# Kernel optimization log

Hardware: AMD Instinct MI355X
Metric: run time of the kernel (lower is better)

The kernel has to match this reference:

```python
import jax, jax.numpy as jnp
import numpy as np

B, TE, TD, HE, HD = 16, 512, 64, 512, 512


def setup_inputs() -> dict:
    key = jax.random.key(0)
    k1, k2, k3, k4, k5 = jax.random.split(key, 5)
    return {
        "encoder_out_seq": jax.random.normal(k1, (B, TE, HE), dtype=jnp.float32),
        "decoder_out_seq": jax.random.normal(k2, (B, TD, HD), dtype=jnp.float32),
        "W_a": jax.random.normal(k3, (HE, HE), dtype=jnp.float32) * 0.05,
        "U_a": jax.random.normal(k4, (HD, HE), dtype=jnp.float32) * 0.05,
        "V_a": jax.random.normal(k5, (HE, 1), dtype=jnp.float32) * 0.05,
    }


def reference(encoder_out_seq, decoder_out_seq, W_a, U_a, V_a):
    # Bahdanau additive attention, batched over all decoder steps at once
    # (the original K.rnn loop over Td is embarrassingly parallel).
    Ws = jnp.einsum('bte,eh->bth', encoder_out_seq, W_a)   # [B,Te,He]
    Uh = jnp.einsum('bdk,kh->bdh', decoder_out_seq, U_a)   # [B,Td,He]
    # additive combine + tanh: [B,Td,Te,He]
    act = jnp.tanh(Ws[:, None, :, :] + Uh[:, :, None, :])
    e = jnp.einsum('bdth,h->bdt', act, V_a[:, 0])          # [B,Td,Te]
    e = jax.nn.softmax(e, axis=-1)                          # attention weights
    c = jnp.einsum('bdt,bth->bdh', e, encoder_out_seq)      # [B,Td,He] context
    return (c, e)
```

## Files before the change

kernel.cpp:

```cpp
#include <hip/hip_runtime.h>
#include <hip/hip_bf16.h>

#define BB 16
#define TE 512
#define TD 64
#define HE 512

#define PRESCALE 2.8853900817779268f

typedef __attribute__((ext_vector_type(8))) short bf16x8;
typedef __attribute__((ext_vector_type(4))) float f32x4;

__device__ __forceinline__ float fexp2(float x) {
#if __has_builtin(__builtin_amdgcn_exp2f)
    return __builtin_amdgcn_exp2f(x);
#else
    return exp2f(x);
#endif
}
__device__ __forceinline__ float frcp(float x) {
#if __has_builtin(__builtin_amdgcn_rcpf)
    return __builtin_amdgcn_rcpf(x);
#else
    return __fdividef(1.f, x);
#endif
}

__device__ __forceinline__ void split2(float x, unsigned short& h, unsigned short& l) {
    __hip_bfloat16 hb = __float2bfloat16(x);
    h = *(unsigned short*)&hb;
    float r = x - __bfloat162float(hb);
    __hip_bfloat16 lb = __float2bfloat16(r);
    l = *(unsigned short*)&lb;
}

__device__ __forceinline__ void gload16(const unsigned short* g, void* l) {
    __builtin_amdgcn_global_load_lds(
        (const __attribute__((address_space(1))) unsigned int*)g,
        (__attribute__((address_space(3))) unsigned int*)l, 16, 0, 0);
}



__device__ __forceinline__ void tile_load(const float* __restrict__ src, int ld,
                                          float (*tile)[64], int tid)
{
#pragma unroll
    for (int p = 0; p < 4; ++p) {
        const int f = p * 256 + tid;
        const int r = f >> 4, c4 = f & 15;
        const float4 v = *(const float4*)&src[(size_t)r * ld + c4 * 4];
        *(float4*)&tile[r][((c4 ^ (r & 7))) << 2] = v;
    }
}

__device__ __forceinline__ void tile_outA(float (*tile)[64],
                                          unsigned short* __restrict__ H,
                                          unsigned short* __restrict__ L,
                                          size_t Ms, size_t sg_base, size_t m_base, int tid)
{
#pragma unroll
    for (int p = 0; p < 2; ++p) {
        const int task = p * 256 + tid;
        const int s = task >> 6, mm = task & 63;
        const float4 x = *(const float4*)&tile[mm][(((s << 1)    ) ^ (mm & 7)) << 2];
        const float4 y = *(const float4*)&tile[mm][(((s << 1) | 1) ^ (mm & 7)) << 2];
        ushort4 ha, la, hb, lb;
        split2(x.x, ha.x, la.x); split2(x.y, ha.y, la.y);
        split2(x.z, ha.z, la.z); split2(x.w, ha.w, la.w);
        split2(y.x, hb.x, lb.x); split2(y.y, hb.y, lb.y);
        split2(y.z, hb.z, lb.z); split2(y.w, hb.w, lb.w);
        const size_t o = ((sg_base + s) * Ms + m_base + mm) * 8;
        *(ushort4*)&H[o] = ha; *(ushort4*)&H[o + 4] = hb;
        *(ushort4*)&L[o] = la; *(ushort4*)&L[o + 4] = lb;
    }
}

__device__ __forceinline__ void tile_outT(float (*tile)[64],
                                          unsigned short* __restrict__ H,
                                          unsigned short* __restrict__ L,
                                          size_t Ns, size_t sg_base, size_t n_base, int tid)
{
#pragma unroll
    for (int p = 0; p < 2; ++p) {
        const int task = p * 256 + tid;
        const int s2 = task >> 6, hh = task & 63;
        float v[8];
#pragma unroll
        for (int q = 0; q < 8; ++q) {
            const int r = s2 * 8 + q;
            v[q] = tile[r][((((hh >> 2)) ^ (r & 7)) << 2) + (hh & 3)];
        }
        ushort4 ha, la, hb, lb;
        split2(v[0], ha.x, la.x); split2(v[1], ha.y, la.y);
        split2(v[2], ha.z, la.z); split2(v[3], ha.w, la.w);
        split2(v[4], hb.x, lb.x); split2(v[5], hb.y, lb.y);
        split2(v[6], hb.z, lb.z); split2(v[7], hb.w, lb.w);
        const size_t o = ((sg_base + s2) * Ns + n_base + hh) * 8;
        *(ushort4*)&H[o] = ha; *(ushort4*)&H[o + 4] = hb;
        *(ushort4*)&L[o] = la; *(ushort4*)&L[o + 4] = lb;
    }
}

__global__ __launch_bounds__(256)
void split_all(const float* __restrict__ enc,
               unsigned short* __restrict__ eAh, unsigned short* __restrict__ eAl,
               unsigned short* __restrict__ eTh, unsigned short* __restrict__ eTl,
               const float* __restrict__ dec,
               unsigned short* __restrict__ dH, unsigned short* __restrict__ dL,
               const float* __restrict__ Wa,
               unsigned short* __restrict__ wH, unsigned short* __restrict__ wL,
               const float* __restrict__ Ua,
               unsigned short* __restrict__ uH, unsigned short* __restrict__ uL)
{
    __shared__ float tile[64][64];
    const int tid = threadIdx.x;
    const int x = blockIdx.x, y = blockIdx.y, z = blockIdx.z;

    if (z < 16) {
        if (y < 8) {
            const int h0 = x * 64, t0 = y * 64;
            const size_t bo = (size_t)z * TE * HE;
            tile_load(enc + bo + (size_t)t0 * HE + h0, HE, tile, tid);
            __syncthreads();
            tile_outA(tile, eAh, eAl, (size_t)BB * TE, h0 >> 3, (size_t)z * TE + t0, tid);
            tile_outT(tile, eTh + bo, eTl + bo, HE, t0 >> 3, h0, tid);
        } else if (y == 8) {
            const int m0 = z * 64, h0 = x * 64;
            tile_load(dec + (size_t)m0 * HE + h0, HE, tile, tid);
            __syncthreads();
            tile_outA(tile, dH, dL, (size_t)BB * TD, h0 >> 3, m0, tid);
        }
        return;
    }
    const int yy = (y < 8) ? y : y - 8;
    const float* X = (y < 8) ? Wa : Ua;
    unsigned short* H = (y < 8) ? wH : uH;
    unsigned short* L = (y < 8) ? wL : uL;
    const int r0 = yy * 64, c0 = x * 64;
    tile_load(X + (size_t)r0 * HE + c0, HE, tile, tid);
    __syncthreads();
    tile_outT(tile, H, L, HE, r0 >> 3, c0, tid);
}

#define GEMM_BODY(AH, AL, BH, BL, CPTR, MM, NN, KK, ROW0, COL0, EPI)          \
    f32x4 acc[4][2];                                                           \
    _Pragma("unroll") for (int mi = 0; mi < 4; ++mi)                           \
        _Pragma("unroll") for (int ni = 0; ni < 2; ++ni)                       \
            acc[mi][ni] = (f32x4){0.f, 0.f, 0.f, 0.f};                         \
    auto STAGE = [&](int buf, int k0) {                                        \
        const int sg = k0 >> 3;                                                \
        _Pragma("unroll") for (int c = 0; c < 2; ++c) {                        \
            const int task = c * 256 + tid;                                    \
            const int g = task >> 7, idx = task & 127;                         \
            int mrow = (ROW0) + idx; if (mrow >= (MM)) mrow -= (MM);           \
            const size_t ao = ((size_t)(sg + g) * (MM) + mrow) * 8;            \
            gload16((AH) + ao, smem[buf] + task * 16);                         \
            gload16((AL) + ao, smem[buf] + 8192 + task * 16);                  \
        }                                                                      \
        {                                                                      \
            const int g = tid >> 6, idx = tid & 63;                            \
            const size_t bo = ((size_t)(sg + g) * (NN) + (COL0) + idx) * 8;    \
            gload16((BH) + bo, smem[buf] + 16384 + tid * 16);                  \
            gload16((BL) + bo, smem[buf] + 20480 + tid * 16);                  \
        }                                                                      \
    };                                                                         \
    STAGE(0, 0);                                                               \
    int buf = 0;                                                               \
    for (int k0 = 0; k0 < (KK); k0 += 32) {                                    \
        if (k0 + 32 < (KK)) {                                                  \
            STAGE(buf ^ 1, k0 + 32);                                           \
            asm volatile("s_waitcnt vmcnt(6)\n\ts_barrier" ::: "memory");      \
        } else {                                                               \
            asm volatile("s_waitcnt vmcnt(0)\n\ts_barrier" ::: "memory");      \
        }                                                                      \
        bf16x8 ah[4], al[4], bh[2], bl[2];                                     \
        _Pragma("unroll") for (int mi = 0; mi < 4; ++mi) {                     \
            const int off = (fg * 128 + wr * 64 + mi * 16 + fr) * 16;          \
            ah[mi] = *(const bf16x8*)(smem[buf] + off);                        \
            al[mi] = *(const bf16x8*)(smem[buf] + 8192 + off);                 \
        }                                                                      \
        _Pragma("unroll") for (int ni = 0; ni < 2; ++ni) {                     \
            const int off = (fg * 64 + wc * 32 + ni * 16 + fr) * 16;           \
            bh[ni] = *(const bf16x8*)(smem[buf] + 16384 + off);                \
            bl[ni] = *(const bf16x8*)(smem[buf] + 20480 + off);                \
        }                                                                      \
        _Pragma("unroll") for (int mi = 0; mi < 4; ++mi)                       \
            _Pragma("unroll") for (int ni = 0; ni < 2; ++ni) {                 \
                acc[mi][ni] = __builtin_amdgcn_mfma_f32_16x16x32_bf16(ah[mi], bh[ni], acc[mi][ni], 0, 0, 0); \
                acc[mi][ni] = __builtin_amdgcn_mfma_f32_16x16x32_bf16(ah[mi], bl[ni], acc[mi][ni], 0, 0, 0); \
                acc[mi][ni] = __builtin_amdgcn_mfma_f32_16x16x32_bf16(al[mi], bh[ni], acc[mi][ni], 0, 0, 0); \
            }                                                                  \
        asm volatile("s_barrier" ::: "memory");                                \
        buf ^= 1;                                                              \
    }                                                                          \
    _Pragma("unroll") for (int mi = 0; mi < 4; ++mi) {                         \
        const int rbase = (ROW0) + wr * 64 + mi * 16 + fg * 4;                 \
        _Pragma("unroll") for (int ni = 0; ni < 2; ++ni) {                     \
            const int col = (COL0) + wc * 32 + ni * 16 + fr;                   \
            _Pragma("unroll") for (int r = 0; r < 4; ++r) {                    \
                const int row = rbase + r;                                     \
                if (row < (MM)) { float val = EPI(acc[mi][ni][r]);             \
                    (CPTR)[(size_t)row * (NN) + col] = val; }                  \
            }                                                                  \
        }                                                                      \
    }

#define EPI_EXP2(v) fexp2((v) * PRESCALE)
#define EPI_ID(v)   (v)

__global__ __launch_bounds__(256)
void gemm_ws_uh(const unsigned short* __restrict__ eAh, const unsigned short* __restrict__ eAl,
                const unsigned short* __restrict__ wBh, const unsigned short* __restrict__ wBl,
                float* __restrict__ Ew,
                const unsigned short* __restrict__ dAh, const unsigned short* __restrict__ dAl,
                const unsigned short* __restrict__ uBh, const unsigned short* __restrict__ uBl,
                float* __restrict__ Eu)
{
    __shared__ char smem[2][24576];
    const int tid  = threadIdx.x;
    const int lane = tid & 63;
    const int wave = tid >> 6;
    const int wr = wave >> 1, wc = wave & 1;
    const int fr = lane & 15, fg = lane >> 4;

    const unsigned short *Ahi, *Alo, *Bhi, *Blo;
    float* C;
    int M, row0;
    if (blockIdx.y < 64) {
        Ahi = eAh; Alo = eAl; Bhi = wBh; Blo = wBl; C = Ew;
        M = BB * TE; row0 = blockIdx.y * 128;
    } else {
        Ahi = dAh; Alo = dAl; Bhi = uBh; Blo = uBl; C = Eu;
        M = BB * TD; row0 = (blockIdx.y - 64) * 128;
    }
    const int N = HE, K = HE;
    const int col0 = blockIdx.x * 64;

    GEMM_BODY(Ahi, Alo, Bhi, Blo, C, M, N, K, row0, col0, EPI_EXP2)
}

__global__ __launch_bounds__(256)
void gemm_ctx(const unsigned short* __restrict__ Ahi_, const unsigned short* __restrict__ Alo_,
              const unsigned short* __restrict__ Bhi_, const unsigned short* __restrict__ Blo_,
              float* __restrict__ C_, int M, int N, int K,
              long long sA, long long sB, long long sC)
{
    __shared__ char smem[2][24576];
    const int tid  = threadIdx.x;
    const int lane = tid & 63;
    const int wave = tid >> 6;
    const int wr = wave >> 1, wc = wave & 1;
    const int fr = lane & 15, fg = lane >> 4;
    const int row0 = blockIdx.y * 128;
    const int col0 = blockIdx.x * 64;

    const unsigned short* Ahi = Ahi_ + (size_t)blockIdx.z * sA;
    const unsigned short* Alo = Alo_ + (size_t)blockIdx.z * sA;
    const unsigned short* Bhi = Bhi_ + (size_t)blockIdx.z * sB;
    const unsigned short* Blo = Blo_ + (size_t)blockIdx.z * sB;
    float* C = C_ + (size_t)blockIdx.z * sC;

    GEMM_BODY(Ahi, Alo, Bhi, Blo, C, M, N, K, row0, col0, EPI_ID)
}

__global__ __launch_bounds__(256)
void gemm_f32(const float* __restrict__ A, const float* __restrict__ Bm,
              float* __restrict__ C, int M, int N, int K,
              long long sAb, long long sBb, long long sCb, float scale, int emode)
{
    __shared__ float As[16][68];
    __shared__ float Bs[16][68];

    const int tid = threadIdx.x;
    const int tx  = tid & 15;
    const int ty  = tid >> 4;
    const int row0 = blockIdx.y * 64;
    const int col0 = blockIdx.x * 64;

    A  += (long long)blockIdx.z * sAb;
    Bm += (long long)blockIdx.z * sBb;
    C  += (long long)blockIdx.z * sCb;

    float acc[4][4] = {};

    for (int k0 = 0; k0 < K; k0 += 16) {
        {
            const int r = tid >> 2;
            const int c = (tid & 3) * 4;
            const float4 av = *(const float4*)&A[(long long)(row0 + r) * K + k0 + c];
            As[c + 0][r] = av.x; As[c + 1][r] = av.y;
            As[c + 2][r] = av.z; As[c + 3][r] = av.w;
        }
        {
            const int r = tid >> 4;
            const int c = (tid & 15) * 4;
            *(float4*)&Bs[r][c] = *(const float4*)&Bm[(long long)(k0 + r) * N + col0 + c];
        }
        __syncthreads();

#pragma unroll
        for (int kk = 0; kk < 16; ++kk) {
            const float4 a = *(const float4*)&As[kk][ty * 4];
            const float4 b = *(const float4*)&Bs[kk][tx * 4];
            acc[0][0] += a.x * b.x; acc[0][1] += a.x * b.y; acc[0][2] += a.x * b.z; acc[0][3] += a.x * b.w;
            acc[1][0] += a.y * b.x; acc[1][1] += a.y * b.y; acc[1][2] += a.y * b.z; acc[1][3] += a.y * b.w;
            acc[2][0] += a.z * b.x; acc[2][1] += a.z * b.y; acc[2][2] += a.z * b.z; acc[2][3] += a.z * b.w;
            acc[3][0] += a.w * b.x; acc[3][1] += a.w * b.y; acc[3][2] += a.w * b.z; acc[3][3] += a.w * b.w;
        }
        __syncthreads();
    }

#pragma unroll
    for (int i = 0; i < 4; ++i) {
        float4 o;
        o.x = acc[i][0] * scale; o.y = acc[i][1] * scale;
        o.z = acc[i][2] * scale; o.w = acc[i][3] * scale;
        if (emode) { o.x = fexp2(o.x); o.y = fexp2(o.y); o.z = fexp2(o.z); o.w = fexp2(o.w); }
        *(float4*)&C[(long long)(row0 + ty * 4 + i) * N + col0 + tx * 4] = o;
    }
}

__global__ __launch_bounds__(256)
void scores_raw(const float* __restrict__ Ew, const float* __restrict__ Eu,
                const float* __restrict__ V, float* __restrict__ part)
{
    __shared__ float Ws_s[32][64];
    __shared__ float Uh_s[32][64];
    __shared__ float Vr_s[HE];

    const int tid = threadIdx.x;
    const int tg  = tid & 7;
    const int dg  = tid >> 3;

    const int tt0  = blockIdx.x * 32;
    const int quar = blockIdx.y & 3;
    const int d0   = (blockIdx.y >> 2) * 32;
    const int b    = blockIdx.z;

    const float* Wsg = Ew + (long long)b * TE * HE;
    const float* Uhg = Eu + ((long long)b * TD + d0) * HE;

    if (tid < 128) {
        const float4 v = *(const float4*)&V[tid * 4];
        float4 o; o.x = -2.f * v.x; o.y = -2.f * v.y; o.z = -2.f * v.z; o.w = -2.f * v.w;
        *(float4*)&Vr_s[tid * 4] = o;
    }

    float acc[4] = {0.f, 0.f, 0.f, 0.f};
    const int wswz = tg & 7;
    const int uswz = dg & 7;
    const int hbase = quar * (HE / 4);

    for (int hc = hbase; hc < hbase + HE / 4; hc += 64) {
        __syncthreads();
#pragma unroll
        for (int k = 0; k < 2; ++k) {
            const int idx = tid + k * 256;
            const int r   = idx >> 4;
            const int c4  = idx & 15;
            const float4 wv = *(const float4*)&Wsg[(long long)(tt0 + r) * HE + hc + c4 * 4];
            *(float4*)&Ws_s[r][(c4 ^ ((r >> 2) & 7)) * 4] = wv;
            const float4 uv = *(const float4*)&Uhg[(long long)r * HE + hc + c4 * 4];
            *(float4*)&Uh_s[r][(c4 ^ (r & 7)) * 4] = uv;
        }
        __syncthreads();

#pragma unroll 4
        for (int hs = 0; hs < 64; hs += 4) {
            const int h4 = hs >> 2;
            const float4 vv = *(const float4*)&Vr_s[hc + hs];
            const float4 u  = *(const float4*)&Uh_s[dg][(h4 ^ uswz) * 4];
#pragma unroll
            for (int i = 0; i < 4; ++i) {
                const float4 w = *(const float4*)&Ws_s[tg * 4 + i][(h4 ^ wswz) * 4];
                acc[i] = fmaf(vv.x, frcp(fmaf(w.x, u.x, 1.f)), acc[i]);
                acc[i] = fmaf(vv.y, frcp(fmaf(w.y, u.y, 1.f)), acc[i]);
                acc[i] = fmaf(vv.z, frcp(fmaf(w.z, u.z, 1.f)), acc[i]);
                acc[i] = fmaf(vv.w, frcp(fmaf(w.w, u.w, 1.f)), acc[i]);
            }
        }
    }

    float* dst = part + (size_t)quar * (BB * TD * TE);
    float4 o; o.x = acc[0]; o.y = acc[1]; o.z = acc[2]; o.w = acc[3];
    *(float4*)&dst[((long long)b * TD + d0 + dg) * TE + tt0 + tg * 4] = o;
}

__global__ __launch_bounds__(256)
void softmax_rows(const float* __restrict__ part, float* __restrict__ e,
                  unsigned short* __restrict__ H, unsigned short* __restrict__ L)
{
    const int lane = threadIdx.x & 63;
    const int wave = threadIdx.x >> 6;
    const long long row = blockIdx.x * 4 + wave;

    float4 a = {0.f, 0.f, 0.f, 0.f}, c = {0.f, 0.f, 0.f, 0.f};
#pragma unroll
    for (int q = 0; q < 4; ++q) {
        const float* p = part + (size_t)q * (BB * TD * TE) + row * TE;
        const float4 aq = *(const float4*)&p[lane * 4];
        const float4 cq = *(const float4*)&p[lane * 4 + 256];
        a.x += aq.x; a.y += aq.y; a.z += aq.z; a.w += aq.w;
        c.x += cq.x; c.y += cq.y; c.z += cq.z; c.w += cq.w;
    }

    float m = fmaxf(fmaxf(fmaxf(a.x, a.y), fmaxf(a.z, a.w)),
                    fmaxf(fmaxf(c.x, c.y), fmaxf(c.z, c.w)));
#pragma unroll
    for (int off = 32; off; off >>= 1) m = fmaxf(m, __shfl_xor(m, off));

    a.x = __expf(a.x - m); a.y = __expf(a.y - m); a.z = __expf(a.z - m); a.w = __expf(a.w - m);
    c.x = __expf(c.x - m); c.y = __expf(c.y - m); c.z = __expf(c.z - m); c.w = __expf(c.w - m);

    float s = (a.x + a.y + a.z + a.w) + (c.x + c.y + c.z + c.w);
#pragma unroll
    for (int off = 32; off; off >>= 1) s += __shfl_xor(s, off);

    const float inv = __fdividef(1.f, s);
    a.x *= inv; a.y *= inv; a.z *= inv; a.w *= inv;
    c.x *= inv; c.y *= inv; c.z *= inv; c.w *= inv;
    float* pe = e + row * TE;
    *(float4*)&pe[lane * 4] = a;
    *(float4*)&pe[lane * 4 + 256] = c;

    if (H) {
        const int b = (int)(row >> 6);
        const int d = (int)(row & 63);
        const size_t base = (size_t)b * (TD * TE);
        ushort4 h, l;
        {
            const int t0 = lane * 4;
            const size_t o = base + ((size_t)(t0 >> 3) * TD + d) * 8 + (t0 & 7);
            split2(a.x, h.x, l.x); split2(a.y, h.y, l.y);
            split2(a.z, h.z, l.z); split2(a.w, h.w, l.w);
            *(ushort4*)&H[o] = h;
            *(ushort4*)&L[o] = l;
        }
        {
            const int t0 = lane * 4 + 256;
            const size_t o = base + ((size_t)(t0 >> 3) * TD + d) * 8 + (t0 & 7);
            split2(c.x, h.x, l.x); split2(c.y, h.y, l.y);
            split2(c.z, h.z, l.z); split2(c.w, h.w, l.w);
            *(ushort4*)&H[o] = h;
            *(ushort4*)&L[o] = l;
        }
    }
}

extern "C" void kernel_launch(void* const* d_in, const int* in_sizes, int n_in,
                              void* d_out, int out_size, void* d_ws, size_t ws_size,
                              hipStream_t stream)
{
    const float* enc = (const float*)d_in[0];
    const float* dec = (const float*)d_in[1];
    const float* Wa  = (const float*)d_in[2];
    const float* Ua  = (const float*)d_in[3];
    const float* Va  = (const float*)d_in[4];

    float* out   = (float*)d_out;
    float* c_out = out;
    float* e_out = out + (size_t)BB * TD * HE;

    char* w = (char*)d_ws;
    float* Ew  = (float*)(w);
    float* Eu  = (float*)(w + 16777216);
    unsigned short* encAh = (unsigned short*)(w + 18874368);
    unsigned short* encAl = (unsigned short*)(w + 27262976);
    unsigned short* encTh = (unsigned short*)(w + 35651584);
    unsigned short* encTl = (unsigned short*)(w + 44040192);
    unsigned short* decAh = (unsigned short*)(w + 52428800);
    unsigned short* decAl = (unsigned short*)(w + 53477376);
    unsigned short* WaTh  = (unsigned short*)(w + 54525952);
    unsigned short* WaTl  = (unsigned short*)(w + 55050240);
    unsigned short* UaTh  = (unsigned short*)(w + 55574528);
    unsigned short* UaTl  = (unsigned short*)(w + 56098816);
    unsigned short* eh    = (unsigned short*)(w + 56623104);
    unsigned short* el    = (unsigned short*)(w + 57671680);
    float* part = (float*)(w + 58720256);
    const size_t REQUIRED = 67108864;

    dim3 blk(256);

    if (ws_size >= REQUIRED) {
        split_all<<<dim3(8, 16, 17), blk, 0, stream>>>(
            enc, encAh, encAl, encTh, encTl,
            dec, decAh, decAl, Wa, WaTh, WaTl, Ua, UaTh, UaTl);

        gemm_ws_uh<<<dim3(8, 72, 1), blk, 0, stream>>>(
            encAh, encAl, WaTh, WaTl, Ew, decAh, decAl, UaTh, UaTl, Eu);

        scores_raw<<<dim3(TE / 32, (TD / 32) * 4, BB), blk, 0, stream>>>(Ew, Eu, Va, part);
        softmax_rows<<<dim3(BB * TD / 4), blk, 0, stream>>>(part, e_out, eh, el);

        gemm_ctx<<<dim3(8, 1, BB), blk, 0, stream>>>(
            eh, el, encTh, encTl, c_out, TD, HE, TE,
            (long long)TD * TE, (long long)TE * HE, (long long)TD * HE);
    } else {
        float* pf = (float*)(w + 18874368);
        gemm_f32<<<dim3(HE / 64, (BB * TE) / 64, 1), blk, 0, stream>>>(
            enc, Wa, Ew, BB * TE, HE, HE, 0, 0, 0, PRESCALE, 1);
        gemm_f32<<<dim3(HE / 64, (BB * TD) / 64, 1), blk, 0, stream>>>(
            dec, Ua, Eu, BB * TD, HE, HE, 0, 0, 0, PRESCALE, 1);
        scores_raw<<<dim3(TE / 32, (TD / 32) * 4, BB), blk, 0, stream>>>(Ew, Eu, Va, pf);
        softmax_rows<<<dim3(BB * TD / 4), blk, 0, stream>>>(pf, e_out, nullptr, nullptr);
        gemm_f32<<<dim3(HE / 64, TD / 64, BB), blk, 0, stream>>>(
            e_out, enc, c_out, TD, HE, TE,
            (long long)TD * TE, (long long)TE * HE, (long long)TD * HE, 1.0f, 0);
    }
}
```

Measured before the change: 90.63 us.

## Fuse all stages into one cooperative persistent kernel with grid syncs

Replaces the five separate launches (split, projection GEMMs, scores, softmax, context GEMM) with a single cooperative persistent kernel. Each stage loops over its tasks by block index, and grid.sync() separates the stages. The GEMM tile shrinks from 128x64 to 64x64 so there are more tiles to spread across the persistent blocks. This removes per-launch overhead and inter-kernel gaps, at the cost of grid-wide barriers and a grid capped by occupancy, which may leave some stages underfilled.

Result: slower. 247.6 us (+173.3%).

```diff
diff --git a/kernel.cpp b/kernel.cpp
--- a/kernel.cpp
+++ b/kernel.cpp
@@ -1,5 +1,8 @@
 #include <hip/hip_runtime.h>
 #include <hip/hip_bf16.h>
+#include <hip/hip_cooperative_groups.h>
+
+namespace cg = cooperative_groups;
 
 #define BB 16
 #define TE 512
@@ -39,7 +42,6 @@
         (const __attribute__((address_space(1))) unsigned int*)g,
         (__attribute__((address_space(3))) unsigned int*)l, 16, 0, 0);
 }
-
 
 
 __device__ __forceinline__ void tile_load(const float* __restrict__ src, int ld,
@@ -102,21 +104,13 @@
     }
 }
 
-__global__ __launch_bounds__(256)
-void split_all(const float* __restrict__ enc,
-               unsigned short* __restrict__ eAh, unsigned short* __restrict__ eAl,
-               unsigned short* __restrict__ eTh, unsigned short* __restrict__ eTl,
-               const float* __restrict__ dec,
-               unsigned short* __restrict__ dH, unsigned short* __restrict__ dL,
-               const float* __restrict__ Wa,
-               unsigned short* __restrict__ wH, unsigned short* __restrict__ wL,
-               const float* __restrict__ Ua,
-               unsigned short* __restrict__ uH, unsigned short* __restrict__ uL)
-{
-    __shared__ float tile[64][64];
-    const int tid = threadIdx.x;
-    const int x = blockIdx.x, y = blockIdx.y, z = blockIdx.z;
-
+__device__ __forceinline__ void split_task(int x, int y, int z, float (*tile)[64], int tid,
+    const float* enc, unsigned short* eAh, unsigned short* eAl,
+    unsigned short* eTh, unsigned short* eTl,
+    const float* dec, unsigned short* dH, unsigned short* dL,
+    const float* Wa, unsigned short* wH, unsigned short* wL,
+    const float* Ua, unsigned short* uH, unsigned short* uL)
+{
     if (z < 16) {
         if (y < 8) {
             const int h0 = x * 64, t0 = y * 64;
@@ -143,209 +137,98 @@
     tile_outT(tile, H, L, HE, r0 >> 3, c0, tid);
 }
 
-#define GEMM_BODY(AH, AL, BH, BL, CPTR, MM, NN, KK, ROW0, COL0, EPI)          \
-    f32x4 acc[4][2];                                                           \
-    _Pragma("unroll") for (int mi = 0; mi < 4; ++mi)                           \
-        _Pragma("unroll") for (int ni = 0; ni < 2; ++ni)                       \
-            acc[mi][ni] = (f32x4){0.f, 0.f, 0.f, 0.f};                         \
-    auto STAGE = [&](int buf, int k0) {                                        \
-        const int sg = k0 >> 3;                                                \
-        _Pragma("unroll") for (int c = 0; c < 2; ++c) {                        \
-            const int task = c * 256 + tid;                                    \
-            const int g = task >> 7, idx = task & 127;                         \
-            int mrow = (ROW0) + idx; if (mrow >= (MM)) mrow -= (MM);           \
-            const size_t ao = ((size_t)(sg + g) * (MM) + mrow) * 8;            \
-            gload16((AH) + ao, smem[buf] + task * 16);                         \
-            gload16((AL) + ao, smem[buf] + 8192 + task * 16);                  \
-        }                                                                      \
-        {                                                                      \
-            const int g = tid >> 6, idx = tid & 63;                            \
-            const size_t bo = ((size_t)(sg + g) * (NN) + (COL0) + idx) * 8;    \
-            gload16((BH) + bo, smem[buf] + 16384 + tid * 16);                  \
-            gload16((BL) + bo, smem[buf] + 20480 + tid * 16);                  \
-        }                                                                      \
-    };                                                                         \
-    STAGE(0, 0);                                                               \
-    int buf = 0;                                                               \
-    for (int k0 = 0; k0 < (KK); k0 += 32) {                                    \
-        if (k0 + 32 < (KK)) {                                                  \
-            STAGE(buf ^ 1, k0 + 32);                                           \
-            asm volatile("s_waitcnt vmcnt(6)\n\ts_barrier" ::: "memory");      \
-        } else {                                                               \
-            asm volatile("s_waitcnt vmcnt(0)\n\ts_barrier" ::: "memory");      \
-        }                                                                      \
-        bf16x8 ah[4], al[4], bh[2], bl[2];                                     \
-        _Pragma("unroll") for (int mi = 0; mi < 4; ++mi) {                     \
-            const int off = (fg * 128 + wr * 64 + mi * 16 + fr) * 16;          \
-            ah[mi] = *(const bf16x8*)(smem[buf] + off);                        \
-            al[mi] = *(const bf16x8*)(smem[buf] + 8192 + off);                 \
-        }                                                                      \
-        _Pragma("unroll") for (int ni = 0; ni < 2; ++ni) {                     \
-            const int off = (fg * 64 + wc * 32 + ni * 16 + fr) * 16;           \
-            bh[ni] = *(const bf16x8*)(smem[buf] + 16384 + off);                \
-            bl[ni] = *(const bf16x8*)(smem[buf] + 20480 + off);                \
-        }                                                                      \
-        _Pragma("unroll") for (int mi = 0; mi < 4; ++mi)                       \
-            _Pragma("unroll") for (int ni = 0; ni < 2; ++ni) {                 \
-                acc[mi][ni] = __builtin_amdgcn_mfma_f32_16x16x32_bf16(ah[mi], bh[ni], acc[mi][ni], 0, 0, 0); \
-                acc[mi][ni] = __builtin_amdgcn_mfma_f32_16x16x32_bf16(ah[mi], bl[ni], acc[mi][ni], 0, 0, 0); \
-                acc[mi][ni] = __builtin_amdgcn_mfma_f32_16x16x32_bf16(al[mi], bh[ni], acc[mi][ni], 0, 0, 0); \
-            }                                                                  \
-        asm volatile("s_barrier" ::: "memory");                                \
-        buf ^= 1;                                                              \
-    }                                                                          \
-    _Pragma("unroll") for (int mi = 0; mi < 4; ++mi) {                         \
-        const int rbase = (ROW0) + wr * 64 + mi * 16 + fg * 4;                 \
-        _Pragma("unroll") for (int ni = 0; ni < 2; ++ni) {                     \
-            const int col = (COL0) + wc * 32 + ni * 16 + fr;                   \
-            _Pragma("unroll") for (int r = 0; r < 4; ++r) {                    \
-                const int row = rbase + r;                                     \
-                if (row < (MM)) { float val = EPI(acc[mi][ni][r]);             \
-                    (CPTR)[(size_t)row * (NN) + col] = val; }                  \
-            }                                                                  \
-        }                                                                      \
-    }
-
-#define EPI_EXP2(v) fexp2((v) * PRESCALE)
-#define EPI_ID(v)   (v)
-
-__global__ __launch_bounds__(256)
-void gemm_ws_uh(const unsigned short* __restrict__ eAh, const unsigned short* __restrict__ eAl,
-                const unsigned short* __restrict__ wBh, const unsigned short* __restrict__ wBl,
-                float* __restrict__ Ew,
-                const unsigned short* __restrict__ dAh, const unsigned short* __restrict__ dAl,
-                const unsigned short* __restrict__ uBh, const unsigned short* __restrict__ uBl,
-                float* __restrict__ Eu)
-{
-    __shared__ char smem[2][24576];
-    const int tid  = threadIdx.x;
+__device__ __forceinline__ void gemm64(char* L,
+    const unsigned short* Ahi, const unsigned short* Alo,
+    const unsigned short* Bhi, const unsigned short* Blo,
+    float* C, int M, int N, int K, int row0, int col0, int emode, int tid)
+{
     const int lane = tid & 63;
     const int wave = tid >> 6;
     const int wr = wave >> 1, wc = wave & 1;
     const int fr = lane & 15, fg = lane >> 4;
 
-    const unsigned short *Ahi, *Alo, *Bhi, *Blo;
-    float* C;
-    int M, row0;
-    if (blockIdx.y < 64) {
-        Ahi = eAh; Alo = eAl; Bhi = wBh; Blo = wBl; C = Ew;
-        M = BB * TE; row0 = blockIdx.y * 128;
-    } else {
-        Ahi = dAh; Alo = dAl; Bhi = uBh; Blo = uBl; C = Eu;
-        M = BB * TD; row0 = (blockIdx.y - 64) * 128;
-    }
-    const int N = HE, K = HE;
-    const int col0 = blockIdx.x * 64;
-
-    GEMM_BODY(Ahi, Alo, Bhi, Blo, C, M, N, K, row0, col0, EPI_EXP2)
-}
-
-__global__ __launch_bounds__(256)
-void gemm_ctx(const unsigned short* __restrict__ Ahi_, const unsigned short* __restrict__ Alo_,
-              const unsigned short* __restrict__ Bhi_, const unsigned short* __restrict__ Blo_,
-              float* __restrict__ C_, int M, int N, int K,
-              long long sA, long long sB, long long sC)
-{
-    __shared__ char smem[2][24576];
-    const int tid  = threadIdx.x;
-    const int lane = tid & 63;
-    const int wave = tid >> 6;
-    const int wr = wave >> 1, wc = wave & 1;
-    const int fr = lane & 15, fg = lane >> 4;
-    const int row0 = blockIdx.y * 128;
-    const int col0 = blockIdx.x * 64;
-
-    const unsigned short* Ahi = Ahi_ + (size_t)blockIdx.z * sA;
-    const unsigned short* Alo = Alo_ + (size_t)blockIdx.z * sA;
-    const unsigned short* Bhi = Bhi_ + (size_t)blockIdx.z * sB;
-    const unsigned short* Blo = Blo_ + (size_t)blockIdx.z * sB;
-    float* C = C_ + (size_t)blockIdx.z * sC;
-
-    GEMM_BODY(Ahi, Alo, Bhi, Blo, C, M, N, K, row0, col0, EPI_ID)
-}
-
-__global__ __launch_bounds__(256)
-void gemm_f32(const float* __restrict__ A, const float* __restrict__ Bm,
-              float* __restrict__ C, int M, int N, int K,
-              long long sAb, long long sBb, long long sCb, float scale, int emode)
-{
-    __shared__ float As[16][68];
-    __shared__ float Bs[16][68];
-
-    const int tid = threadIdx.x;
-    const int tx  = tid & 15;
-    const int ty  = tid >> 4;
-    const int row0 = blockIdx.y * 64;
-    const int col0 = blockIdx.x * 64;
-
-    A  += (long long)blockIdx.z * sAb;
-    Bm += (long long)blockIdx.z * sBb;
-    C  += (long long)blockIdx.z * sCb;
-
-    float acc[4][4] = {};
-
-    for (int k0 = 0; k0 < K; k0 += 16) {
-        {
-            const int r = tid >> 2;
-            const int c = (tid & 3) * 4;
-            const float4 av = *(const float4*)&A[(long long)(row0 + r) * K + k0 + c];
-            As[c + 0][r] = av.x; As[c + 1][r] = av.y;
-            As[c + 2][r] = av.z; As[c + 3][r] = av.w;
-        }
-        {
-            const int r = tid >> 4;
-            const int c = (tid & 15) * 4;
-            *(float4*)&Bs[r][c] = *(const float4*)&Bm[(long long)(k0 + r) * N + col0 + c];
-        }
-        __syncthreads();
-
-#pragma unroll
-        for (int kk = 0; kk < 16; ++kk) {
-            const float4 a = *(const float4*)&As[kk][ty * 4];
-            const float4 b = *(const float4*)&Bs[kk][tx * 4];
-            acc[0][0] += a.x * b.x; acc[0][1] += a.x * b.y; acc[0][2] += a.x * b.z; acc[0][3] += a.x * b.w;
-            acc[1][0] += a.y * b.x; acc[1][1] += a.y * b.y; acc[1][2] += a.y * b.z; acc[1][3] += a.y * b.w;
-            acc[2][0] += a.z * b.x; acc[2][1] += a.z * b.y; acc[2][2] += a.z * b.z; acc[2][3] += a.z * b.w;
-            acc[3][0] += a.w * b.x; acc[3][1] += a.w * b.y; acc[3][2] += a.w * b.z; acc[3][3] += a.w * b.w;
-        }
-        __syncthreads();
-    }
-
-#pragma unroll
-    for (int i = 0; i < 4; ++i) {
-        float4 o;
-        o.x = acc[i][0] * scale; o.y = acc[i][1] * scale;
-        o.z = acc[i][2] * scale; o.w = acc[i][3] * scale;
-        if (emode) { o.x = fexp2(o.x); o.y = fexp2(o.y); o.z = fexp2(o.z); o.w = fexp2(o.w); }
-        *(float4*)&C[(long long)(row0 + ty * 4 + i) * N + col0 + tx * 4] = o;
-    }
-}
-
-__global__ __launch_bounds__(256)
-void scores_raw(const float* __restrict__ Ew, const float* __restrict__ Eu,
-                const float* __restrict__ V, float* __restrict__ part)
-{
-    __shared__ float Ws_s[32][64];
-    __shared__ float Uh_s[32][64];
-    __shared__ float Vr_s[HE];
-
-    const int tid = threadIdx.x;
-    const int tg  = tid & 7;
-    const int dg  = tid >> 3;
-
-    const int tt0  = blockIdx.x * 32;
-    const int quar = blockIdx.y & 3;
-    const int d0   = (blockIdx.y >> 2) * 32;
-    const int b    = blockIdx.z;
-
+    f32x4 acc[2][2];
+#pragma unroll
+    for (int mi = 0; mi < 2; ++mi)
+#pragma unroll
+        for (int ni = 0; ni < 2; ++ni)
+            acc[mi][ni] = (f32x4){0.f, 0.f, 0.f, 0.f};
+
+    auto STAGE = [&](int buf, int k0) {
+        const int sg = k0 >> 3;
+        const int g = tid >> 6, idx = tid & 63;
+        char* sb = L + buf * 16384;
+        int mrow = row0 + idx; if (mrow >= M) mrow -= M;
+        const size_t ao = ((size_t)(sg + g) * M + mrow) * 8;
+        const size_t bo = ((size_t)(sg + g) * N + col0 + idx) * 8;
+        gload16(Ahi + ao, sb + tid * 16);
+        gload16(Alo + ao, sb + 4096 + tid * 16);
+        gload16(Bhi + bo, sb + 8192 + tid * 16);
+        gload16(Blo + bo, sb + 12288 + tid * 16);
+    };
+
+    STAGE(0, 0);
+    int buf = 0;
+    for (int k0 = 0; k0 < K; k0 += 32) {
+        if (k0 + 32 < K) {
+            STAGE(buf ^ 1, k0 + 32);
+            asm volatile("s_waitcnt vmcnt(4)\n\ts_barrier" ::: "memory");
+        } else {
+            asm volatile("s_waitcnt vmcnt(0)\n\ts_barrier" ::: "memory");
+        }
+        char* sb = L + buf * 16384;
+        bf16x8 ah[2], al[2], bh[2], bl[2];
+#pragma unroll
+        for (int mi = 0; mi < 2; ++mi) {
+            const int off = (fg * 64 + wr * 32 + mi * 16 + fr) * 16;
+            ah[mi] = *(const bf16x8*)(sb + off);
+            al[mi] = *(const bf16x8*)(sb + 4096 + off);
+        }
+#pragma unroll
+        for (int ni = 0; ni < 2; ++ni) {
+            const int off = (fg * 64 + wc * 32 + ni * 16 + fr) * 16;
+            bh[ni] = *(const bf16x8*)(sb + 8192 + off);
+            bl[ni] = *(const bf16x8*)(sb + 12288 + off);
+        }
+#pragma unroll
+        for (int mi = 0; mi < 2; ++mi)
+#pragma unroll
+            for (int ni = 0; ni < 2; ++ni) {
+                acc[mi][ni] = __builtin_amdgcn_mfma_f32_16x16x32_bf16(ah[mi], bh[ni], acc[mi][ni], 0, 0, 0);
+                acc[mi][ni] = __builtin_amdgcn_mfma_f32_16x16x32_bf16(ah[mi], bl[ni], acc[mi][ni], 0, 0, 0);
+                acc[mi][ni] = __builtin_amdgcn_mfma_f32_16x16x32_bf16(al[mi], bh[ni], acc[mi][ni], 0, 0, 0);
+            }
+        asm volatile("s_barrier" ::: "memory");
+        buf ^= 1;
+    }
+
+#pragma unroll
+    for (int mi = 0; mi < 2; ++mi) {
+        const int rbase = row0 + wr * 32 + mi * 16 + fg * 4;
+#pragma unroll
+        for (int ni = 0; ni < 2; ++ni) {
+            const int col = col0 + wc * 32 + ni * 16 + fr;
+#pragma unroll
+            for (int r = 0; r < 4; ++r) {
+                const int row = rbase + r;
+                if (row < M) {
+                    float val = acc[mi][ni][r];
+                    if (emode) val = fexp2(val * PRESCALE);
+                    C[(size_t)row * N + col] = val;
+                }
+            }
+        }
+    }
+}
+
+__device__ __forceinline__ void scores_task(float (*Ws_s)[64], float (*Uh_s)[64],
+    const float* Vr_s, int tt0, int quar, int d0, int b,
+    const float* Ew, const float* Eu, float* part, int tid)
+{
+    const int tg = tid & 7;
+    const int dg = tid >> 3;
     const float* Wsg = Ew + (long long)b * TE * HE;
     const float* Uhg = Eu + ((long long)b * TD + d0) * HE;
-
-    if (tid < 128) {
-        const float4 v = *(const float4*)&V[tid * 4];
-        float4 o; o.x = -2.f * v.x; o.y = -2.f * v.y; o.z = -2.f * v.z; o.w = -2.f * v.w;
-        *(float4*)&Vr_s[tid * 4] = o;
-    }
 
     float acc[4] = {0.f, 0.f, 0.f, 0.f};
     const int wswz = tg & 7;
@@ -387,13 +270,10 @@
     *(float4*)&dst[((long long)b * TD + d0 + dg) * TE + tt0 + tg * 4] = o;
 }
 
-__global__ __launch_bounds__(256)
-void softmax_rows(const float* __restrict__ part, float* __restrict__ e,
-                  unsigned short* __restrict__ H, unsigned short* __restrict__ L)
-{
-    const int lane = threadIdx.x & 63;
-    const int wave = threadIdx.x >> 6;
-    const long long row = blockIdx.x * 4 + wave;
+__device__ __forceinline__ void softmax_task(long long row, const float* part,
+    float* e, unsigned short* H, unsigned short* L, int tid)
+{
+    const int lane = tid & 63;
 
     float4 a = {0.f, 0.f, 0.f, 0.f}, c = {0.f, 0.f, 0.f, 0.f};
 #pragma unroll
@@ -424,27 +304,226 @@
     *(float4*)&pe[lane * 4] = a;
     *(float4*)&pe[lane * 4 + 256] = c;
 
-    if (H) {
-        const int b = (int)(row >> 6);
-        const int d = (int)(row & 63);
-        const size_t base = (size_t)b * (TD * TE);
-        ushort4 h, l;
+    const int b = (int)(row >> 6);
+    const int d = (int)(row & 63);
+    const size_t base = (size_t)b * (TD * TE);
+    ushort4 h, l;
+    {
+        const int t0 = lane * 4;
+        const size_t o = base + ((size_t)(t0 >> 3) * TD + d) * 8 + (t0 & 7);
+        split2(a.x, h.x, l.x); split2(a.y, h.y, l.y);
+        split2(a.z, h.z, l.z); split2(a.w, h.w, l.w);
+        *(ushort4*)&H[o] = h;
+        *(ushort4*)&L[o] = l;
+    }
+    {
+        const int t0 = lane * 4 + 256;
+        const size_t o = base + ((size_t)(t0 >> 3) * TD + d) * 8 + (t0 & 7);
+        split2(c.x, h.x, l.x); split2(c.y, h.y, l.y);
+        split2(c.z, h.z, l.z); split2(c.w, h.w, l.w);
+        *(ushort4*)&H[o] = h;
+        *(ushort4*)&L[o] = l;
+    }
+}
+
+__global__ __launch_bounds__(256)
+void mega(const float* enc, const float* dec, const float* Wa, const float* Ua,
+          const float* Va, float* out, char* w)
+{
+    __shared__ __align__(16) char L[32768];
+    cg::grid_group grid = cg::this_grid();
+    const int tid  = threadIdx.x;
+    const int nblk = gridDim.x;
+
+    float* Ew  = (float*)(w);
+    float* Eu  = (float*)(w + 16777216);
+    unsigned short* encAh = (unsigned short*)(w + 18874368);
+    unsigned short* encAl = (unsigned short*)(w + 27262976);
+    unsigned short* encTh = (unsigned short*)(w + 35651584);
+    unsigned short* encTl = (unsigned short*)(w + 44040192);
+    unsigned short* decAh = (unsigned short*)(w + 52428800);
+    unsigned short* decAl = (unsigned short*)(w + 53477376);
+    unsigned short* WaTh  = (unsigned short*)(w + 54525952);
+    unsigned short* WaTl  = (unsigned short*)(w + 55050240);
+    unsigned short* UaTh  = (unsigned short*)(w + 55574528);
+    unsigned short* UaTl  = (unsigned short*)(w + 56098816);
+    unsigned short* eh    = (unsigned short*)(w + 56623104);
+    unsigned short* el    = (unsigned short*)(w + 57671680);
+    float* part  = (float*)(w + 58720256);
+    float* c_out = out;
+    float* e_out = out + (size_t)BB * TD * HE;
+
+    {
+        float (*tile)[64] = (float(*)[64])L;
+        for (int t = blockIdx.x; t < 2176; t += nblk) {
+            __syncthreads();
+            const int z = t >> 7, rem = t & 127;
+            const int y = rem >> 3, x = rem & 7;
+            split_task(x, y, z, tile, tid, enc, encAh, encAl, encTh, encTl,
+                       dec, decAh, decAl, Wa, WaTh, WaTl, Ua, UaTh, UaTl);
+        }
+    }
+    grid.sync();
+
+    for (int t = blockIdx.x; t < 1152; t += nblk) {
+        if (t < 1024) {
+            gemm64(L, encAh, encAl, WaTh, WaTl, Ew, BB * TE, HE, HE,
+                   (t >> 3) * 64, (t & 7) * 64, 1, tid);
+        } else {
+            const int tt = t - 1024;
+            gemm64(L, decAh, decAl, UaTh, UaTl, Eu, BB * TD, HE, HE,
+                   (tt >> 3) * 64, (tt & 7) * 64, 1, tid);
+        }
+    }
+    grid.sync();
+
+    {
+        float (*Ws_s)[64] = (float(*)[64])L;
+        float (*Uh_s)[64] = (float(*)[64])(L + 8192);
+        float* Vr_s = (float*)(L + 16384);
+        if (tid < 128) {
+            const float4 v = *(const float4*)&Va[tid * 4];
+            float4 o; o.x = -2.f * v.x; o.y = -2.f * v.y; o.z = -2.f * v.z; o.w = -2.f * v.w;
+            *(float4*)&Vr_s[tid * 4] = o;
+        }
+        for (int t = blockIdx.x; t < 2048; t += nblk) {
+            const int x = t & 15, y = (t >> 4) & 7, z = t >> 7;
+            scores_task(Ws_s, Uh_s, Vr_s, x * 32, y & 3, (y >> 2) * 32, z,
+                        Ew, Eu, part, tid);
+        }
+    }
+    grid.sync();
+
+    for (int t = blockIdx.x; t < 256; t += nblk) {
+        const long long row = (long long)t * 4 + (tid >> 6);
+        softmax_task(row, part, e_out, eh, el, tid);
+    }
+    grid.sync();
+
+    for (int t = blockIdx.x; t < 128; t += nblk) {
+        const int b = t >> 3, ct = t & 7;
+        gemm64(L, eh + (size_t)b * TD * TE, el + (size_t)b * TD * TE,
+               encTh + (size_t)b * TE * HE, encTl + (size_t)b * TE * HE,
+               c_out + (size_t)b * TD * HE, TD, HE, TE, 0, ct * 64, 0, tid);
+    }
+}
+
+__global__ __launch_bounds__(256)
+void split_all(const float* __restrict__ enc,
+               unsigned short* __restrict__ eAh, unsigned short* __restrict__ eAl,
+               unsigned short* __restrict__ eTh, unsigned short* __restrict__ eTl,
+               const float* __restrict__ dec,
+               unsigned short* __restrict__ dH, unsigned short* __restrict__ dL,
+               const float* __restrict__ Wa,
+               unsigned short* __restrict__ wH, unsigned short* __restrict__ wL,
+               const float* __restrict__ Ua,
+               unsigned short* __restrict__ uH, unsigned short* __restrict__ uL)
+{
+    __shared__ float tile[64][64];
+    split_task(blockIdx.x, blockIdx.y, blockIdx.z, tile, threadIdx.x,
+               enc, eAh, eAl, eTh, eTl, dec, dH, dL, Wa, wH, wL, Ua, uH, uL);
+}
+
+__global__ __launch_bounds__(256)
+void gemm_ws_uh(const unsigned short* __restrict__ eAh, const unsigned short* __restrict__ eAl,
+                const unsigned short* __restrict__ wBh, const unsigned short* __restrict__ wBl,
+                float* __restrict__ Ew,
+                const unsigned short* __restrict__ dAh, const unsigned short* __restrict__ dAl,
+                const unsigned short* __restrict__ uBh, const unsigned short* __restrict__ uBl,
+                float* __restrict__ Eu)
+{
+    __shared__ __align__(16) char L[32768];
+    const int t = blockIdx.y * 8 + blockIdx.x;
+    if (t < 1024)
+        gemm64(L, eAh, eAl, wBh, wBl, Ew, BB * TE, HE, HE,
+               (t >> 3) * 64, (t & 7) * 64, 1, threadIdx.x);
+    else {
+        const int tt = t - 1024;
+        gemm64(L, dAh, dAl, uBh, uBl, Eu, BB * TD, HE, HE,
+               (tt >> 3) * 64, (tt & 7) * 64, 1, threadIdx.x);
+    }
+}
+
+__global__ __launch_bounds__(256)
+void gemm_ctx(const unsigned short* __restrict__ eh, const unsigned short* __restrict__ el,
+              const unsigned short* __restrict__ eTh, const unsigned short* __restrict__ eTl,
+              float* __restrict__ C)
+{
+    __shared__ __align__(16) char L[32768];
+    const int b = blockIdx.z, ct = blockIdx.x;
+    gemm64(L, eh + (size_t)b * TD * TE, el + (size_t)b * TD * TE,
+           eTh + (size_t)b * TE * HE, eTl + (size_t)b * TE * HE,
+           C + (size_t)b * TD * HE, TD, HE, TE, 0, ct * 64, 0, threadIdx.x);
+}
+
+__global__ __launch_bounds__(256)
+void scores_raw(const float* __restrict__ Ew, const float* __restrict__ Eu,
+                const float* __restrict__ V, float* __restrict__ part)
+{
+    __shared__ float Ws_s[32][64];
+    __shared__ float Uh_s[32][64];
+    __shared__ float Vr_s[HE];
+    const int tid = threadIdx.x;
+    if (tid < 128) {
+        const float4 v = *(const float4*)&V[tid * 4];
+        float4 o; o.x = -2.f * v.x; o.y = -2.f * v.y; o.z = -2.f * v.z; o.w = -2.f * v.w;
+        *(float4*)&Vr_s[tid * 4] = o;
+    }
+    scores_task(Ws_s, Uh_s, Vr_s, blockIdx.x * 32, blockIdx.y & 3,
+                (blockIdx.y >> 2) * 32, blockIdx.z, Ew, Eu, part, tid);
+}
+
+__global__ __launch_bounds__(256)
+void softmax_rows(const float* __restrict__ part, float* __restrict__ e,
+                  unsigned short* __restrict__ H, unsigned short* __restrict__ L)
+{
+    const long long row = (long long)blockIdx.x * 4 + (threadIdx.x >> 6);
+    softmax_task(row, part, e, H, L, threadIdx.x);
+}
+
+__global__ __launch_bounds__(256)
+void gemm_f32(const float* __restrict__ A, const float* __restrict__ Bm,
+              float* __restrict__ C, int M, int N, int K,
+              long long sAb, long long sBb, long long sCb, float scale, int emode)
+{
+    __shared__ float As[16][68];
+    __shared__ float Bs[16][68];
+    const int tid = threadIdx.x;
+    const int tx = tid & 15, ty = tid >> 4;
+    const int row0 = blockIdx.y * 64, col0 = blockIdx.x * 64;
+    A += (long long)blockIdx.z * sAb; Bm += (long long)blockIdx.z * sBb;
+    C += (long long)blockIdx.z * sCb;
+    float acc[4][4] = {};
+    for (int k0 = 0; k0 < K; k0 += 16) {
         {
-            const int t0 = lane * 4;
-            const size_t o = base + ((size_t)(t0 >> 3) * TD + d) * 8 + (t0 & 7);
-            split2(a.x, h.x, l.x); split2(a.y, h.y, l.y);
-            split2(a.z, h.z, l.z); split2(a.w, h.w, l.w);
-            *(ushort4*)&H[o] = h;
-            *(ushort4*)&L[o] = l;
+            const int r = tid >> 2, c = (tid & 3) * 4;
+            const float4 av = *(const float4*)&A[(long long)(row0 + r) * K + k0 + c];
+            As[c + 0][r] = av.x; As[c + 1][r] = av.y;
+            As[c + 2][r] = av.z; As[c + 3][r] = av.w;
         }
         {
-            const int t0 = lane * 4 + 256;
-            const size_t o = base + ((size_t)(t0 >> 3) * TD + d) * 8 + (t0 & 7);
-            split2(c.x, h.x, l.x); split2(c.y, h.y, l.y);
-            split2(c.z, h.z, l.z); split2(c.w, h.w, l.w);
-            *(ushort4*)&H[o] = h;
-            *(ushort4*)&L[o] = l;
-        }
+            const int r = tid >> 4, c = (tid & 15) * 4;
+            *(float4*)&Bs[r][c] = *(const float4*)&Bm[(long long)(k0 + r) * N + col0 + c];
+        }
+        __syncthreads();
+#pragma unroll
+        for (int kk = 0; kk < 16; ++kk) {
+            const float4 a = *(const float4*)&As[kk][ty * 4];
+            const float4 b = *(const float4*)&Bs[kk][tx * 4];
+            acc[0][0] += a.x * b.x; acc[0][1] += a.x * b.y; acc[0][2] += a.x * b.z; acc[0][3] += a.x * b.w;
+            acc[1][0] += a.y * b.x; acc[1][1] += a.y * b.y; acc[1][2] += a.y * b.z; acc[1][3] += a.y * b.w;
+            acc[2][0] += a.z * b.x; acc[2][1] += a.z * b.y; acc[2][2] += a.z * b.z; acc[2][3] += a.z * b.w;
+            acc[3][0] += a.w * b.x; acc[3][1] += a.w * b.y; acc[3][2] += a.w * b.z; acc[3][3] += a.w * b.w;
+        }
+        __syncthreads();
+    }
+#pragma unroll
+    for (int i = 0; i < 4; ++i) {
+        float4 o;
+        o.x = acc[i][0] * scale; o.y = acc[i][1] * scale;
+        o.z = acc[i][2] * scale; o.w = acc[i][3] * scale;
+        if (emode) { o.x = fexp2(o.x); o.y = fexp2(o.y); o.z = fexp2(o.z); o.w = fexp2(o.w); }
+        *(float4*)&C[(long long)(row0 + ty * 4 + i) * N + col0 + tx * 4] = o;
     }
 }
 
@@ -482,20 +561,27 @@
 
     dim3 blk(256);
 
-    if (ws_size >= REQUIRED) {
+    int coop = 0, dev = 0;
+    hipGetDevice(&dev);
+    hipDeviceGetAttribute(&coop, hipDeviceAttributeCooperativeLaunch, dev);
+    int maxblk = 0;
+    hipOccupancyMaxActiveBlocksPerMultiprocessor(&maxblk, mega, 256, (size_t)0);
+
+    if (ws_size >= REQUIRED && coop && maxblk >= 1) {
+        int G = maxblk * 256;
+        if (G > 2048) G = 2048;
+        void* args[] = {(void*)&enc, (void*)&dec, (void*)&Wa, (void*)&Ua,
+                        (void*)&Va, (void*)&out, (void*)&w};
+        hipLaunchCooperativeKernel(mega, dim3(G), blk, args, 0u, stream);
+    } else if (ws_size >= REQUIRED) {
         split_all<<<dim3(8, 16, 17), blk, 0, stream>>>(
             enc, encAh, encAl, encTh, encTl,
             dec, decAh, decAl, Wa, WaTh, WaTl, Ua, UaTh, UaTl);
-
-        gemm_ws_uh<<<dim3(8, 72, 1), blk, 0, stream>>>(
+        gemm_ws_uh<<<dim3(8, 144, 1), blk, 0, stream>>>(
             encAh, encAl, WaTh, WaTl, Ew, decAh, decAl, UaTh, UaTl, Eu);
-
         scores_raw<<<dim3(TE / 32, (TD / 32) * 4, BB), blk, 0, stream>>>(Ew, Eu, Va, part);
         softmax_rows<<<dim3(BB * TD / 4), blk, 0, stream>>>(part, e_out, eh, el);
-
-        gemm_ctx<<<dim3(8, 1, BB), blk, 0, stream>>>(
-            eh, el, encTh, encTl, c_out, TD, HE, TE,
-            (long long)TD * TE, (long long)TE * HE, (long long)TD * HE);
+        gemm_ctx<<<dim3(8, 1, BB), blk, 0, stream>>>(eh, el, encTh, encTl, c_out);
     } else {
         float* pf = (float*)(w + 18874368);
         gemm_f32<<<dim3(HE / 64, (BB * TE) / 64, 1), blk, 0, stream>>>(
```
